# Kernel tuning notes

Measured on AMD Instinct MI355X. Metric: run time of the kernel, lower is better.

The kernel has to match this reference:

```python
import jax, jax.numpy as jnp
import numpy as np

EPS = 1e-5
DN = ('NCHW', 'OIHW', 'NCHW')


def conv3x3(x, w, b):
    y = jax.lax.conv_general_dilated(x, w, window_strides=(1, 1), padding='SAME',
                                     dimension_numbers=DN)
    return y + b[None, :, None, None]


def bn_relu(x, g, be, m, v):
    # inference-mode BatchNorm2d followed by ReLU, folded into one FMA
    inv = g / jnp.sqrt(v + EPS)
    return jax.nn.relu(x * inv[None, :, None, None] + (be - m * inv)[None, :, None, None])


def haar_idwt2(cA, cH, cV, cD):
    # pywt.idwt2(coeffs, 'db1'): cH = detail along rows (axis -2), cV = detail along cols (axis -1)
    # Exact Haar synthesis -> 2x2 pixel blocks (pixel-shuffle style, no CPU round-trip)
    p00 = (cA + cH + cV + cD) * 0.5  # (2i,   2j)
    p01 = (cA + cH - cV - cD) * 0.5  # (2i,   2j+1)
    p10 = (cA - cH + cV - cD) * 0.5  # (2i+1, 2j)
    p11 = (cA - cH - cV + cD) * 0.5  # (2i+1, 2j+1)
    B, C, H, W = cA.shape
    even = jnp.stack([p00, p01], axis=-1).reshape(B, C, H, 2 * W)
    odd = jnp.stack([p10, p11], axis=-1).reshape(B, C, H, 2 * W)
    return jnp.stack([even, odd], axis=-2).reshape(B, C, 2 * H, 2 * W)


def setup_inputs() -> dict:
    key = jax.random.key(0)
    ks = jax.random.split(key, 24)
    B, IN_C, OUT_C, H, W = 16, 128, 64, 64, 64
    d = {}
    d['x'] = jax.random.normal(ks[0], (B, IN_C, H, W), jnp.float32)
    d['s'] = jax.random.normal(ks[1], (B, OUT_C, 2 * H, 2 * W), jnp.float32)
    # input_convdwt: Conv(in_c -> 4*in_c) + BN
    d['w1'] = jax.random.normal(ks[2], (4 * IN_C, IN_C, 3, 3), jnp.float32) * 0.05
    d['b1'] = jax.random.normal(ks[3], (4 * IN_C,), jnp.float32) * 0.05
    d['g1'] = jax.random.uniform(ks[4], (4 * IN_C,), jnp.float32, 0.5, 1.5)
    d['be1'] = jax.random.normal(ks[5], (4 * IN_C,), jnp.float32) * 0.05
    d['m1'] = jax.random.normal(ks[6], (4 * IN_C,), jnp.float32) * 0.05
    d['v1'] = jax.random.uniform(ks[7], (4 * IN_C,), jnp.float32, 0.5, 1.5)
    # s_con: Conv(in_c -> out_c) + BN
    d['ws'] = jax.random.normal(ks[8], (OUT_C, IN_C, 3, 3), jnp.float32) * 0.05
    d['bs'] = jax.random.normal(ks[9], (OUT_C,), jnp.float32) * 0.05
    d['gs'] = jax.random.uniform(ks[10], (OUT_C,), jnp.float32, 0.5, 1.5)
    d['bes'] = jax.random.normal(ks[11], (OUT_C,), jnp.float32) * 0.05
    d['ms'] = jax.random.normal(ks[12], (OUT_C,), jnp.float32) * 0.05
    d['vs'] = jax.random.uniform(ks[13], (OUT_C,), jnp.float32, 0.5, 1.5)
    # conv: Conv(in_c -> out_c) + BN (applied to concat(s, s_out))
    d['w2'] = jax.random.normal(ks[14], (OUT_C, IN_C, 3, 3), jnp.float32) * 0.05
    d['b2'] = jax.random.normal(ks[15], (OUT_C,), jnp.float32) * 0.05
    d['g2'] = jax.random.uniform(ks[16], (OUT_C,), jnp.float32, 0.5, 1.5)
    d['be2'] = jax.random.normal(ks[17], (OUT_C,), jnp.float32) * 0.05
    d['m2'] = jax.random.normal(ks[18], (OUT_C,), jnp.float32) * 0.05
    d['v2'] = jax.random.uniform(ks[19], (OUT_C,), jnp.float32, 0.5, 1.5)
    return d


def reference(x, s, w1, b1, g1, be1, m1, v1,
              ws, bs, gs, bes, ms, vs,
              w2, b2, g2, be2, m2, v2):
    # input_convdwt: conv -> BN -> ReLU, channels in_c -> 4*in_c
    h = bn_relu(conv3x3(x, w1, b1), g1, be1, m1, v1)
    c = h.shape[1]
    q = c // 4
    cA, cH, cV, cD = h[:, :q], h[:, q:2 * q], h[:, 2 * q:3 * q], h[:, 3 * q:]
    idwt_out = haar_idwt2(cA, cH, cV, cD)  # (B, in_c, 2H, 2W)
    # skip-connection branch (s is not None)
    s_out = bn_relu(conv3x3(idwt_out, ws, bs), gs, bes, ms, vs)  # (B, out_c, 2H, 2W)
    concat = jnp.concatenate([s, s_out], axis=1)                  # (B, in_c, 2H, 2W)
    decoder_output = bn_relu(conv3x3(concat, w2, b2), g2, be2, m2, v2)
    return decoder_output
```

## Files before the change

kernel.cpp:

```cpp
#include <hip/hip_runtime.h>
#include <hip/hip_bf16.h>

typedef __attribute__((ext_vector_type(8))) short short8;
typedef __attribute__((ext_vector_type(4))) float f32x4;
typedef unsigned short u16;

#define EPSV 1e-5f

__device__ __forceinline__ u16 f2bf(float f) {
    __hip_bfloat16 h = __float2bfloat16(f);
    return *reinterpret_cast<u16*>(&h);
}

#define GLOAD_LDS16(g, l)                                                      \
    __builtin_amdgcn_global_load_lds(                                          \
        (const __attribute__((address_space(1))) void*)(g),                    \
        (__attribute__((address_space(3))) void*)(l), 16, 0, 0)

__global__ void cvt_kernel(const float* __restrict__ src, u16* __restrict__ dst,
                           int C, int H, int W, int units) {
    int u = blockIdx.x * 256 + threadIdx.x;
    if (u >= units) return;
    int kb = u & 3;
    int p  = u >> 2;
    int x  = p % W;  p /= W;
    int y  = p % H;  p /= H;
    int n  = p & 15;
    int cc = p >> 4;
    short8 v;
#pragma unroll
    for (int j = 0; j < 8; ++j)
        v[j] = (short)f2bf(src[(((size_t)n * C + cc * 32 + kb * 8 + j) * H + y) * W + x]);
    *(short8*)(dst + ((((size_t)cc * 16 + n) * H + y) * W + x) * 32 + kb * 8) = v;
}

__global__ void repack_w1_kernel(const float* __restrict__ w1, u16* __restrict__ wf) {
    int u = blockIdx.x * 256 + threadIdx.x;
    if (u >= 4 * 8 * 9 * 4 * 64) return;
    int l = u & 63;
    int r = u >> 6;
    int ciC = r & 3;  r >>= 2;
    int t   = r % 9;  r /= 9;
    int bt  = r & 7;
    int cc  = r >> 3;
    int co  = (bt >> 1) * 128 + cc * 32 + (bt & 1) * 16 + (l & 15);
    int ci0 = ciC * 32 + (l >> 4) * 8;
    short8 v;
#pragma unroll
    for (int e = 0; e < 8; ++e)
        v[e] = (short)f2bf(w1[((size_t)co * 128 + ci0 + e) * 9 + t]);
    *(short8*)(wf + (size_t)u * 8) = v;
}

__global__ void repack_wg_kernel(const float* __restrict__ w, u16* __restrict__ wf) {
    int u = blockIdx.x * 256 + threadIdx.x;
    if (u >= 4 * 9 * 4 * 64) return;
    int l = u & 63;
    int r = u >> 6;
    int ciC = r & 3;  r >>= 2;
    int t   = r % 9;
    int bt  = r / 9;
    int co  = bt * 16 + (l & 15);
    int ci0 = ciC * 32 + (l >> 4) * 8;
    short8 v;
#pragma unroll
    for (int e = 0; e < 8; ++e)
        v[e] = (short)f2bf(w[((size_t)co * 128 + ci0 + e) * 9 + t]);
    *(short8*)(wf + (size_t)u * 8) = v;
}

__global__ __launch_bounds__(256, 2)
void conv1_mfma_kernel(const u16* __restrict__ inb, const u16* __restrict__ wf,
                       const float* __restrict__ bb, const float* __restrict__ gg,
                       const float* __restrict__ bee, const float* __restrict__ mm,
                       const float* __restrict__ vv, u16* __restrict__ ob) {
    const int tile = blockIdx.x;
    const int cc   = blockIdx.y;
    const int n    = blockIdx.z;
    const int x0   = (tile & 3) * 16;
    const int y0   = (tile >> 2) * 8;
    const int tid  = threadIdx.x;
    const int lane = tid & 63;
    const int wid  = tid >> 6;
    const int wm   = wid >> 1;
    const int wc   = wid & 1;
    const int kb   = lane >> 4;
    const int xl   = lane & 15;

    __shared__ float4 lds4[720];
    __shared__ float4 wlds[2][1536];
    const short8* ldsr  = (const short8*)lds4;
    const short8* wldsr = (const short8*)wlds;

    f32x4 acc[4][4];
#pragma unroll
    for (int j = 0; j < 4; ++j)
#pragma unroll
        for (int q = 0; q < 4; ++q) acc[j][q] = (f32x4){0.f, 0.f, 0.f, 0.f};

    float4 sreg[3];
    auto load_stage = [&](int ciC) {
#pragma unroll
        for (int p = 0; p < 3; ++p) {
            int e = p * 256 + tid;
            float4 v = make_float4(0.f, 0.f, 0.f, 0.f);
            if (e < 720) {
                int pix = e >> 2, ke = e & 3;
                int yy = pix / 18;
                int xx = pix - yy * 18;
                int gy = y0 - 1 + yy, gx = x0 - 1 + xx;
                if ((unsigned)gy < 64u && (unsigned)gx < 64u)
                    v = *(const float4*)(inb + ((((size_t)ciC * 16 + n) * 64 + gy) * 64 + gx) * 32 + ke * 8);
            }
            sreg[p] = v;
        }
    };
    auto write_stage = [&]() {
#pragma unroll
        for (int p = 0; p < 3; ++p) {
            int e = p * 256 + tid;
            if (e < 720) lds4[e ^ ((e >> 2) & 7)] = sreg[p];
        }
    };
    auto stage_w = [&](int ciC, int dx, int buf) {
#pragma unroll
        for (int i = 0; i < 6; ++i) {
            int seg = wid * 6 + i;
            int bt  = seg / 3;
            int dy  = seg - bt * 3;
            int t   = dy * 3 + dx;
            const u16* gp = wf + (size_t)((cc * 8 + bt) * 9 + t) * 2048 + ciC * 512 + lane * 8;
            GLOAD_LDS16(gp, &wlds[buf][seg * 64]);
        }
    };

    load_stage(0);
    stage_w(0, 0, 0);
    for (int ciC = 0; ciC < 4; ++ciC) {
        write_stage();
        asm volatile("s_waitcnt lgkmcnt(0)" ::: "memory");
        __builtin_amdgcn_s_barrier();
        __builtin_amdgcn_sched_barrier(0);
        if (ciC < 3) load_stage(ciC + 1);
#pragma unroll
        for (int dx = 0; dx < 3; ++dx) {
            const int cur = (ciC + dx) & 1;
            if (dx == 0) {
                if (ciC < 3) asm volatile("s_waitcnt vmcnt(3)" ::: "memory");
                else         asm volatile("s_waitcnt vmcnt(0)" ::: "memory");
            } else {
                asm volatile("s_waitcnt vmcnt(0)" ::: "memory");
            }
            __builtin_amdgcn_sched_barrier(0);
            __builtin_amdgcn_s_barrier();
            __builtin_amdgcn_sched_barrier(0);
            if (dx < 2)        stage_w(ciC, dx + 1, cur ^ 1);
            else if (ciC < 3)  stage_w(ciC + 1, 0, cur ^ 1);

            short8 a[6];
#pragma unroll
            for (int r = 0; r < 6; ++r) {
                int pix = (wm * 4 + r) * 18 + xl + dx;
                int e = pix * 4 + kb;
                a[r] = ldsr[e ^ ((e >> 2) & 7)];
            }
#pragma unroll
            for (int dy = 0; dy < 3; ++dy) {
                short8 b[4];
#pragma unroll
                for (int q = 0; q < 4; ++q) {
                    int bt = q * 2 + wc;
                    b[q] = wldsr[cur * 1536 + (bt * 3 + dy) * 64 + lane];
                }
#pragma unroll
                for (int j = 0; j < 4; ++j)
#pragma unroll
                    for (int q = 0; q < 4; ++q)
                        acc[j][q] = __builtin_amdgcn_mfma_f32_16x16x32_bf16(a[j + dy], b[q], acc[j][q], 0, 0, 0);
            }
        }
        __builtin_amdgcn_s_barrier();
    }

    float invq[4], shq[4];
#pragma unroll
    for (int q = 0; q < 4; ++q) {
        int co  = q * 128 + cc * 32 + wc * 16 + xl;
        float inv = gg[co] / sqrtf(vv[co] + EPSV);
        invq[q] = inv;
        shq[q]  = bb[co] * inv + bee[co] - mm[co] * inv;
    }
    const int c32 = wc * 16 + xl;
#pragma unroll
    for (int j = 0; j < 4; ++j) {
        int y = y0 + wm * 4 + j;
#pragma unroll
        for (int i = 0; i < 4; ++i) {
            float A_ = fmaxf(acc[j][0][i] * invq[0] + shq[0], 0.f);
            float H_ = fmaxf(acc[j][1][i] * invq[1] + shq[1], 0.f);
            float V_ = fmaxf(acc[j][2][i] * invq[2] + shq[2], 0.f);
            float D_ = fmaxf(acc[j][3][i] * invq[3] + shq[3], 0.f);
            float p00 = (A_ + H_ + V_ + D_) * 0.5f;
            float p01 = (A_ + H_ - V_ - D_) * 0.5f;
            float p10 = (A_ - H_ + V_ - D_) * 0.5f;
            float p11 = (A_ - H_ - V_ + D_) * 0.5f;
            int oy = 2 * y, ox = 2 * (x0 + kb * 4 + i);
            size_t base = ((((size_t)cc * 16 + n) * 128 + oy) * 128 + ox) * 32 + c32;
            ob[base]            = f2bf(p00);
            ob[base + 32]       = f2bf(p01);
            ob[base + 128 * 32] = f2bf(p10);
            ob[base + 128 * 32 + 32] = f2bf(p11);
        }
    }
}

template <bool FP32OUT>
__global__ __launch_bounds__(256, 2)
void convg_mfma_kernel(const u16* __restrict__ inb, const u16* __restrict__ wf,
                       const float* __restrict__ bb, const float* __restrict__ gg,
                       const float* __restrict__ bee, const float* __restrict__ mm,
                       const float* __restrict__ vv, u16* __restrict__ ob,
                       float* __restrict__ of) {
    const int tile = blockIdx.x;
    const int n    = blockIdx.y;
    const int x0   = (tile & 7) * 16;
    const int y0   = (tile >> 3) * 8;
    const int tid  = threadIdx.x;
    const int lane = tid & 63;
    const int wid  = tid >> 6;
    const int wm   = wid >> 1;
    const int wc   = wid & 1;
    const int kb   = lane >> 4;
    const int xl   = lane & 15;

    __shared__ float4 lds4[720];
    const short8* ldsr = (const short8*)lds4;

    f32x4 acc[4][2];
#pragma unroll
    for (int j = 0; j < 4; ++j)
#pragma unroll
        for (int cb = 0; cb < 2; ++cb) acc[j][cb] = (f32x4){0.f, 0.f, 0.f, 0.f};

    float4 sreg[3];
    auto load_stage = [&](int ciC) {
#pragma unroll
        for (int p = 0; p < 3; ++p) {
            int e = p * 256 + tid;
            float4 v = make_float4(0.f, 0.f, 0.f, 0.f);
            if (e < 720) {
                int pix = e >> 2, ke = e & 3;
                int yy = pix / 18;
                int xx = pix - yy * 18;
                int gy = y0 - 1 + yy, gx = x0 - 1 + xx;
                if ((unsigned)gy < 128u && (unsigned)gx < 128u)
                    v = *(const float4*)(inb + ((((size_t)ciC * 16 + n) * 128 + gy) * 128 + gx) * 32 + ke * 8);
            }
            sreg[p] = v;
        }
    };
    auto write_stage = [&]() {
#pragma unroll
        for (int p = 0; p < 3; ++p) {
            int e = p * 256 + tid;
            if (e < 720) lds4[e ^ ((e >> 2) & 7)] = sreg[p];
        }
    };

    load_stage(0);
    for (int ciC = 0; ciC < 4; ++ciC) {
        write_stage();
        __syncthreads();
        if (ciC < 3) load_stage(ciC + 1);
#pragma unroll
        for (int dx = 0; dx < 3; ++dx) {
            short8 a[6];
#pragma unroll
            for (int r = 0; r < 6; ++r) {
                int pix = (wm * 4 + r) * 18 + xl + dx;
                int e = pix * 4 + kb;
                a[r] = ldsr[e ^ ((e >> 2) & 7)];
            }
#pragma unroll
            for (int dy = 0; dy < 3; ++dy) {
                const int t = dy * 3 + dx;
                short8 b[2];
#pragma unroll
                for (int cb = 0; cb < 2; ++cb) {
                    int bt = wc * 2 + cb;
                    b[cb] = *(const short8*)(wf + ((size_t)((bt * 9 + t) * 4 + ciC) * 64 + lane) * 8);
                }
#pragma unroll
                for (int j = 0; j < 4; ++j)
#pragma unroll
                    for (int cb = 0; cb < 2; ++cb)
                        acc[j][cb] = __builtin_amdgcn_mfma_f32_16x16x32_bf16(a[j + dy], b[cb], acc[j][cb], 0, 0, 0);
            }
        }
        __syncthreads();
    }

#pragma unroll
    for (int cb = 0; cb < 2; ++cb) {
        int co = (wc * 2 + cb) * 16 + xl;
        float inv = gg[co] / sqrtf(vv[co] + EPSV);
        float sh  = bb[co] * inv + bee[co] - mm[co] * inv;
#pragma unroll
        for (int j = 0; j < 4; ++j) {
            int y = y0 + wm * 4 + j;
            if (FP32OUT) {
                float4 v4;
                v4.x = fmaxf(acc[j][cb][0] * inv + sh, 0.f);
                v4.y = fmaxf(acc[j][cb][1] * inv + sh, 0.f);
                v4.z = fmaxf(acc[j][cb][2] * inv + sh, 0.f);
                v4.w = fmaxf(acc[j][cb][3] * inv + sh, 0.f);
                *(float4*)&of[(((size_t)n * 64 + co) * 128 + y) * 128 + x0 + kb * 4] = v4;
            } else {
#pragma unroll
                for (int i = 0; i < 4; ++i) {
                    float val = fmaxf(acc[j][cb][i] * inv + sh, 0.f);
                    int xg = x0 + kb * 4 + i;
                    ob[((((size_t)(co >> 5) * 16 + n) * 128 + y) * 128 + xg) * 32 + (co & 31)] = f2bf(val);
                }
            }
        }
    }
}

extern "C" void kernel_launch(void* const* d_in, const int* in_sizes, int n_in,
                              void* d_out, int out_size, void* d_ws, size_t ws_size,
                              hipStream_t stream) {
    const float* x   = (const float*)d_in[0];
    const float* s   = (const float*)d_in[1];
    const float* w1  = (const float*)d_in[2];
    const float* b1  = (const float*)d_in[3];
    const float* g1  = (const float*)d_in[4];
    const float* be1 = (const float*)d_in[5];
    const float* m1  = (const float*)d_in[6];
    const float* v1  = (const float*)d_in[7];
    const float* wsw = (const float*)d_in[8];
    const float* bs  = (const float*)d_in[9];
    const float* gs  = (const float*)d_in[10];
    const float* bes = (const float*)d_in[11];
    const float* ms  = (const float*)d_in[12];
    const float* vs  = (const float*)d_in[13];
    const float* w2  = (const float*)d_in[14];
    const float* b2  = (const float*)d_in[15];
    const float* g2  = (const float*)d_in[16];
    const float* be2 = (const float*)d_in[17];
    const float* m2  = (const float*)d_in[18];
    const float* v2  = (const float*)d_in[19];
    float* out = (float*)d_out;

    char* wsp = (char*)d_ws;
    u16* xb   = (u16*)(wsp);
    u16* idwt = (u16*)(wsp + 16777216);
    u16* cat  = (u16*)(wsp + 16777216 + 67108864);
    u16* wf1  = (u16*)(wsp + 16777216 + 67108864 + 67108864);
    u16* wfS  = (u16*)(wsp + 16777216 + 67108864 + 67108864 + 1179648);
    u16* wf2  = (u16*)(wsp + 16777216 + 67108864 + 67108864 + 1179648 + 147456);

    cvt_kernel<<<dim3(4096), dim3(256), 0, stream>>>(x, xb, 128, 64, 64, 1048576);
    cvt_kernel<<<dim3(8192), dim3(256), 0, stream>>>(s, cat, 64, 128, 128, 2097152);
    repack_w1_kernel<<<dim3(288), dim3(256), 0, stream>>>(w1, wf1);
    repack_wg_kernel<<<dim3(36), dim3(256), 0, stream>>>(wsw, wfS);
    repack_wg_kernel<<<dim3(36), dim3(256), 0, stream>>>(w2, wf2);

    conv1_mfma_kernel<<<dim3(32, 4, 16), dim3(256), 0, stream>>>(
        xb, wf1, b1, g1, be1, m1, v1, idwt);

    convg_mfma_kernel<false><<<dim3(128, 16), dim3(256), 0, stream>>>(
        idwt, wfS, bs, gs, bes, ms, vs, cat + (size_t)2 * 16 * 128 * 128 * 32, nullptr);

    convg_mfma_kernel<true><<<dim3(128, 16), dim3(256), 0, stream>>>(
        cat, wf2, b2, g2, be2, m2, v2, nullptr, out);
}
```

Measured before the change: 213.2 us.

## Fuse skip-tensor conversion into final conv and stage weights in LDS

Removes the separate conversion kernel for the skip tensor s. The final conv now reads fp32 s directly, with strided per-channel loads, and converts it to bf16 while loading the first two channel chunks. It also double-buffers the weight fragments in LDS via global_load_lds and replaces the syncthreads with explicit waitcnt and barriers, so weight fetches overlap the MFMA work. The cost is uncoalesced scalar fp32 loads of s, which get reread by neighbouring tiles, plus more LDS use that may reduce occupancy.

New measurement: 213.8 us. About the same (+0.3%).

```diff
diff --git a/kernel.cpp b/kernel.cpp
--- a/kernel.cpp
+++ b/kernel.cpp
@@ -214,9 +214,10 @@
     }
 }
 
-template <bool FP32OUT>
+template <bool FP32OUT, bool SFUSE>
 __global__ __launch_bounds__(256, 2)
-void convg_mfma_kernel(const u16* __restrict__ inb, const u16* __restrict__ wf,
+void convg_mfma_kernel(const u16* __restrict__ inb, const float* __restrict__ sfp,
+                       const u16* __restrict__ wf,
                        const float* __restrict__ bb, const float* __restrict__ gg,
                        const float* __restrict__ bee, const float* __restrict__ mm,
                        const float* __restrict__ vv, u16* __restrict__ ob,
@@ -234,7 +235,9 @@
     const int xl   = lane & 15;
 
     __shared__ float4 lds4[720];
-    const short8* ldsr = (const short8*)lds4;
+    __shared__ float4 wlds[2][768];
+    const short8* ldsr  = (const short8*)lds4;
+    const short8* wldsr = (const short8*)wlds;
 
     f32x4 acc[4][2];
 #pragma unroll
@@ -253,8 +256,19 @@
                 int yy = pix / 18;
                 int xx = pix - yy * 18;
                 int gy = y0 - 1 + yy, gx = x0 - 1 + xx;
-                if ((unsigned)gy < 128u && (unsigned)gx < 128u)
+                bool ib = (unsigned)gy < 128u && (unsigned)gx < 128u;
+                if (SFUSE && ciC < 2) {
+                    if (ib) {
+                        const float* sp = sfp + (((size_t)n * 64 + ciC * 32 + ke * 8) * 128 + gy) * 128 + gx;
+                        short8 sv;
+#pragma unroll
+                        for (int j = 0; j < 8; ++j)
+                            sv[j] = (short)f2bf(sp[(size_t)j * 16384]);
+                        v = *(float4*)&sv;
+                    }
+                } else if (ib) {
                     v = *(const float4*)(inb + ((((size_t)ciC * 16 + n) * 128 + gy) * 128 + gx) * 32 + ke * 8);
+                }
             }
             sreg[p] = v;
         }
@@ -266,14 +280,36 @@
             if (e < 720) lds4[e ^ ((e >> 2) & 7)] = sreg[p];
         }
     };
+    auto stage_w = [&](int ciC, int dx, int buf) {
+#pragma unroll
+        for (int i = 0; i < 3; ++i) {
+            int seg = wid * 3 + i;
+            int bt  = seg / 3;
+            int dy  = seg - bt * 3;
+            int t   = dy * 3 + dx;
+            const u16* gp = wf + (size_t)(((bt * 9 + t) * 4 + ciC) * 64 + lane) * 8;
+            GLOAD_LDS16(gp, &wlds[buf][seg * 64]);
+        }
+    };
 
     load_stage(0);
+    stage_w(0, 0, 0);
     for (int ciC = 0; ciC < 4; ++ciC) {
         write_stage();
-        __syncthreads();
-        if (ciC < 3) load_stage(ciC + 1);
+        asm volatile("s_waitcnt lgkmcnt(0)" ::: "memory");
+        __builtin_amdgcn_s_barrier();
+        __builtin_amdgcn_sched_barrier(0);
 #pragma unroll
         for (int dx = 0; dx < 3; ++dx) {
+            const int cur = (ciC + dx) & 1;
+            asm volatile("s_waitcnt vmcnt(0)" ::: "memory");
+            __builtin_amdgcn_sched_barrier(0);
+            __builtin_amdgcn_s_barrier();
+            __builtin_amdgcn_sched_barrier(0);
+            if (dx < 2)        stage_w(ciC, dx + 1, cur ^ 1);
+            else if (ciC < 3)  stage_w(ciC + 1, 0, cur ^ 1);
+            if (dx == 0 && ciC < 3) load_stage(ciC + 1);
+
             short8 a[6];
 #pragma unroll
             for (int r = 0; r < 6; ++r) {
@@ -283,12 +319,11 @@
             }
 #pragma unroll
             for (int dy = 0; dy < 3; ++dy) {
-                const int t = dy * 3 + dx;
                 short8 b[2];
 #pragma unroll
                 for (int cb = 0; cb < 2; ++cb) {
                     int bt = wc * 2 + cb;
-                    b[cb] = *(const short8*)(wf + ((size_t)((bt * 9 + t) * 4 + ciC) * 64 + lane) * 8);
+                    b[cb] = wldsr[cur * 768 + (bt * 3 + dy) * 64 + lane];
                 }
 #pragma unroll
                 for (int j = 0; j < 4; ++j)
@@ -297,7 +332,7 @@
                         acc[j][cb] = __builtin_amdgcn_mfma_f32_16x16x32_bf16(a[j + dy], b[cb], acc[j][cb], 0, 0, 0);
             }
         }
-        __syncthreads();
+        __builtin_amdgcn_s_barrier();
     }
 
 #pragma unroll
@@ -361,7 +396,6 @@
     u16* wf2  = (u16*)(wsp + 16777216 + 67108864 + 67108864 + 1179648 + 147456);
 
     cvt_kernel<<<dim3(4096), dim3(256), 0, stream>>>(x, xb, 128, 64, 64, 1048576);
-    cvt_kernel<<<dim3(8192), dim3(256), 0, stream>>>(s, cat, 64, 128, 128, 2097152);
     repack_w1_kernel<<<dim3(288), dim3(256), 0, stream>>>(w1, wf1);
     repack_wg_kernel<<<dim3(36), dim3(256), 0, stream>>>(wsw, wfS);
     repack_wg_kernel<<<dim3(36), dim3(256), 0, stream>>>(w2, wf2);
@@ -369,9 +403,10 @@
     conv1_mfma_kernel<<<dim3(32, 4, 16), dim3(256), 0, stream>>>(
         xb, wf1, b1, g1, be1, m1, v1, idwt);
 
-    convg_mfma_kernel<false><<<dim3(128, 16), dim3(256), 0, stream>>>(
-        idwt, wfS, bs, gs, bes, ms, vs, cat + (size_t)2 * 16 * 128 * 128 * 32, nullptr);
-
-    convg_mfma_kernel<true><<<dim3(128, 16), dim3(256), 0, stream>>>(
-        cat, wf2, b2, g2, be2, m2, v2, nullptr, out);
-}
+    convg_mfma_kernel<false, false><<<dim3(128, 16), dim3(256), 0, stream>>>(
+        idwt, nullptr, wfS, bs, gs, bes, ms, vs,
+        cat + (size_t)2 * 16 * 128 * 128 * 32, nullptr);
+
+    convg_mfma_kernel<true, true><<<dim3(128, 16), dim3(256), 0, stream>>>(
+        cat, s, wf2, b2, g2, be2, m2, v2, nullptr, out);
+}
```
